# Kernel tuning notes

Measured on AMD Instinct MI355X. Metric: run time of the kernel, lower is better.

The kernel has to match this reference:

```python
import jax, jax.numpy as jnp
import numpy as np

H = 16
D_MODEL = 1024
D_K = D_MODEL // H


def setup_inputs() -> dict:
    key = jax.random.key(0)
    kx, kq, kk, kv, ko = jax.random.split(key, 5)
    B, T = 4, 2048
    scale = 1.0 / np.sqrt(D_MODEL)
    return {
        "X": jax.random.normal(kx, (B, T, D_MODEL), dtype=jnp.float32),
        "W_q": jax.random.normal(kq, (D_MODEL, D_MODEL), dtype=jnp.float32) * scale,
        "W_k": jax.random.normal(kk, (D_MODEL, D_MODEL), dtype=jnp.float32) * scale,
        "W_v": jax.random.normal(kv, (D_MODEL, D_MODEL), dtype=jnp.float32) * scale,
        "W_o": jax.random.normal(ko, (D_MODEL, D_MODEL), dtype=jnp.float32) * scale,
    }


def reference(X, W_q, W_k, W_v, W_o):
    B, T, D = X.shape
    # projections (torch Linear: x @ W.T); weights stored as [out, in]=[D,D]
    Q = (X @ W_q.T).reshape(B, T, H, D_K).transpose(0, 2, 1, 3)  # [B,H,T,Dk]
    K = (X @ W_k.T).reshape(B, T, H, D_K).transpose(0, 2, 1, 3)
    V = (X @ W_v.T).reshape(B, T, H, D_K).transpose(0, 2, 1, 3)
    S = jnp.einsum("bhqd,bhkd->bhqk", Q, K) * (D_K ** -0.5)  # [B,H,T,T]
    causal = jnp.tril(jnp.ones((T, T), dtype=bool))
    S = jnp.where(causal, S, -jnp.inf)
    A = jax.nn.softmax(S, axis=-1)
    out = jnp.einsum("bhqk,bhkd->bhqd", A, V)  # [B,H,T,Dk]
    out = out.transpose(0, 2, 1, 3).reshape(B, T, D)
    return out @ W_o.T
```

## Files before the change

### kernel.cpp

```cpp
#include <hip/hip_runtime.h>
#include <hip/hip_bf16.h>

#define T_SEQ 2048
#define NB 4
#define NH 16
#define DK 64
#define DM 1024
#define QKS 2048

typedef __attribute__((ext_vector_type(8))) __bf16 bf16x8;
typedef __attribute__((ext_vector_type(4))) __bf16 bf16x4;
typedef __attribute__((ext_vector_type(4))) float f32x4;
typedef __attribute__((ext_vector_type(2))) int i32x2;
typedef __attribute__((ext_vector_type(4))) int i32x4;

__device__ __forceinline__ void gl_lds16(const __bf16* g, __bf16* l) {
  __builtin_amdgcn_global_load_lds(
      (const __attribute__((address_space(1))) void*)g,
      (__attribute__((address_space(3))) void*)l,
      16, 0, 0);
}

__device__ __forceinline__ unsigned cvt_pk_bf16(float lo, float hi) {
  unsigned r;
  asm("v_cvt_pk_bf16_f32 %0, %1, %2" : "=v"(r) : "v"(lo), "v"(hi));
  return r;
}

__global__ __launch_bounds__(256) void cast_f32_to_bf16(const float* __restrict__ in,
                                                        __bf16* __restrict__ out, int n4) {
  int i = blockIdx.x * 256 + threadIdx.x;
  if (i >= n4) return;
  float4 v = reinterpret_cast<const float4*>(in)[i];
  bf16x4 o;
  o[0] = (__bf16)v.x; o[1] = (__bf16)v.y; o[2] = (__bf16)v.z; o[3] = (__bf16)v.w;
  reinterpret_cast<bf16x4*>(out)[i] = o;
}

__global__ __launch_bounds__(256) void cast_weights(const float* __restrict__ a,
                                                    const float* __restrict__ b,
                                                    const float* __restrict__ c,
                                                    const float* __restrict__ d,
                                                    __bf16* __restrict__ oa,
                                                    __bf16* __restrict__ ob,
                                                    __bf16* __restrict__ oc,
                                                    __bf16* __restrict__ od) {
  const int which = blockIdx.y;
  const float* in = (which == 0) ? a : (which == 1) ? b : (which == 2) ? c : d;
  __bf16* out = (which == 0) ? oa : (which == 1) ? ob : (which == 2) ? oc : od;
  int i = blockIdx.x * 256 + threadIdx.x;
  float4 v = reinterpret_cast<const float4*>(in)[i];
  bf16x4 o;
  o[0] = (__bf16)v.x; o[1] = (__bf16)v.y; o[2] = (__bf16)v.z; o[3] = (__bf16)v.w;
  reinterpret_cast<bf16x4*>(out)[i] = o;
}

template<typename CT, int MODE>
__global__ __launch_bounds__(256, 2) void gemm_nt(const __bf16* __restrict__ A,
                                                  const __bf16* __restrict__ B,
                                                  CT* __restrict__ C,
                                                  int M, int N, int K) {
  __shared__ alignas(16) __bf16 As[128][64];
  __shared__ alignas(16) __bf16 Bs[128][64];
  const int tid = threadIdx.x;
  const int m0 = blockIdx.y * 128, n0 = blockIdx.x * 128;
  const int w = tid >> 6, l = tid & 63, lg = l >> 4, lr = l & 15;
  const int wr = (w >> 1) * 64, wc = (w & 1) * 64;
  const int srow = l >> 3;
  const int schunk = (l & 7) ^ srow;

  f32x4 acc[4][4] = {};
  const int rsw = lr & 7;

  for (int k0 = 0; k0 < K; k0 += 64) {
    __syncthreads();
    #pragma unroll
    for (int j = 0; j < 4; ++j) {
      const int rbase = (w * 4 + j) * 8;
      gl_lds16(A + (size_t)(m0 + rbase + srow) * K + k0 + schunk * 8, &As[rbase][0]);
      gl_lds16(B + (size_t)(n0 + rbase + srow) * K + k0 + schunk * 8, &Bs[rbase][0]);
    }
    asm volatile("s_waitcnt vmcnt(0)" ::: "memory");
    __syncthreads();
    #pragma unroll
    for (int kk = 0; kk < 2; ++kk) {
      bf16x8 af[4], bfr[4];
      #pragma unroll
      for (int mt = 0; mt < 4; ++mt) {
        const char* p = (const char*)&As[wr + mt * 16 + lr][0];
        af[mt] = *reinterpret_cast<const bf16x8*>(p + (((kk * 4 + lg) ^ rsw) << 4));
      }
      #pragma unroll
      for (int nt = 0; nt < 4; ++nt) {
        const char* p = (const char*)&Bs[wc + nt * 16 + lr][0];
        bfr[nt] = *reinterpret_cast<const bf16x8*>(p + (((kk * 4 + lg) ^ rsw) << 4));
      }
      __builtin_amdgcn_s_setprio(1);
      #pragma unroll
      for (int mt = 0; mt < 4; ++mt)
        #pragma unroll
        for (int nt = 0; nt < 4; ++nt)
          acc[mt][nt] = __builtin_amdgcn_mfma_f32_16x16x32_bf16(af[mt], bfr[nt], acc[mt][nt], 0, 0, 0);
      __builtin_amdgcn_s_setprio(0);
    }
  }
  const float qsc = (MODE == 1 && n0 < 1024) ? 0.18033688f : 1.0f;
  #pragma unroll
  for (int mt = 0; mt < 4; ++mt)
    #pragma unroll
    for (int nt = 0; nt < 4; ++nt)
      #pragma unroll
      for (int r = 0; r < 4; ++r) {
        const int mg = m0 + wr + mt * 16 + 4 * lg + r;
        int ng = n0 + wc + nt * 16 + lr;
        if (MODE == 2)
          ng = (ng & ~31) | (8 * (lr >> 2) + (lr & 3) + ((nt & 1) << 2));
        float v = acc[mt][nt][r];
        if (MODE == 1) v *= qsc;
        C[(size_t)mg * N + ng] = (CT)v;
      }
}

__global__ __launch_bounds__(256, 3) void attn_fwd(const __bf16* __restrict__ QK,
                                                   const __bf16* __restrict__ VT,
                                                   __bf16* __restrict__ AO) {
  __shared__ alignas(16) __bf16 Ks[2][64][64];
  __shared__ alignas(16) __bf16 Vs[2][64][64];
  const int tid = threadIdx.x;
  const int w = tid >> 6, l = tid & 63, lg = l >> 4, lr = l & 15;

  const int fl = (int)blockIdx.x + 16 * (int)blockIdx.y;
  const int bh = ((fl & 7) << 3) | ((fl >> 3) & 7);
  const int qpair = fl >> 6;
  const int b = bh >> 4, h = bh & 15;
  const size_t bT = (size_t)b * T_SEQ;
  const int M = NB * T_SEQ;

  const int srow = l >> 3;
  const int schunk = (l & 7) ^ srow;
  const __bf16* Kg = QK + bT * QKS + 1024 + h * DK;
  const __bf16* Vg = VT + (size_t)(h * DK) * M + bT;
  const int rsw = lr & 7;

  const int qbA = qpair, qbB = 31 - qpair;
  const int qrwA = qbA * 64 + w * 16, qrwB = qbB * 64 + w * 16;
  const int klastA = qbA * 64, klastB = qbB * 64;

  const __bf16* QpA = QK + (bT + qrwA + lr) * QKS + h * DK;
  const __bf16* QpB = QK + (bT + qrwB + lr) * QKS + h * DK;
  const bf16x8 qfA0 = *reinterpret_cast<const bf16x8*>(QpA + 8 * lg);
  const bf16x8 qfA1 = *reinterpret_cast<const bf16x8*>(QpA + 32 + 8 * lg);
  const bf16x8 qfB0 = *reinterpret_cast<const bf16x8*>(QpB + 8 * lg);
  const bf16x8 qfB1 = *reinterpret_cast<const bf16x8*>(QpB + 32 + 8 * lg);

  f32x4 o_accA[4] = {}, o_accB[4] = {};
  float lsumA = 0.f, lsumB = 0.f;

  auto STAGE = [&](int buf, int kbase) {
    #pragma unroll
    for (int i = 0; i < 2; ++i) {
      const int seg = w * 2 + i;
      gl_lds16(Kg + (size_t)(kbase + seg * 8 + srow) * QKS + schunk * 8,
               &Ks[buf][seg * 8][0]);
      gl_lds16(Vg + (size_t)(seg * 8 + srow) * M + kbase + schunk * 8,
               &Vs[buf][seg * 8][0]);
    }
  };

  auto CHUNK = [&](const bf16x8& qf0, const bf16x8& qf1, f32x4* o_acc,
                   float& lsum, int qrw, bool masked, int k0,
                   const bf16x8* kf, const bf16x8* vf) {
    f32x4 s[4] = {};
    __builtin_amdgcn_s_setprio(1);
    #pragma unroll
    for (int ct = 0; ct < 4; ++ct) {
      s[ct] = __builtin_amdgcn_mfma_f32_16x16x32_bf16(kf[2 * ct], qf0, s[ct], 0, 0, 0);
      s[ct] = __builtin_amdgcn_mfma_f32_16x16x32_bf16(kf[2 * ct + 1], qf1, s[ct], 0, 0, 0);
    }
    __builtin_amdgcn_s_setprio(0);
    if (masked) {
      #pragma unroll
      for (int ct = 0; ct < 4; ++ct)
        #pragma unroll
        for (int r = 0; r < 4; ++r)
          if (k0 + 16 * ct + 4 * lg + r > qrw + lr) s[ct][r] = -1e30f;
    }
    unsigned pk[4][2];
    #pragma unroll
    for (int ct = 0; ct < 4; ++ct) {
      float p0 = exp2f(s[ct][0]), p1 = exp2f(s[ct][1]);
      float p2 = exp2f(s[ct][2]), p3 = exp2f(s[ct][3]);
      lsum += (p0 + p1) + (p2 + p3);
      pk[ct][0] = cvt_pk_bf16(p0, p1);
      pk[ct][1] = cvt_pk_bf16(p2, p3);
    }
    const bf16x8 pf0 = __builtin_bit_cast(bf16x8, i32x4{(int)pk[0][0], (int)pk[0][1],
                                                        (int)pk[1][0], (int)pk[1][1]});
    const bf16x8 pf1 = __builtin_bit_cast(bf16x8, i32x4{(int)pk[2][0], (int)pk[2][1],
                                                        (int)pk[3][0], (int)pk[3][1]});
    __builtin_amdgcn_s_setprio(1);
    #pragma unroll
    for (int dt = 0; dt < 4; ++dt) {
      o_acc[dt] = __builtin_amdgcn_mfma_f32_16x16x32_bf16(pf0, vf[2 * dt],     o_acc[dt], 0, 0, 0);
      o_acc[dt] = __builtin_amdgcn_mfma_f32_16x16x32_bf16(pf1, vf[2 * dt + 1], o_acc[dt], 0, 0, 0);
    }
    __builtin_amdgcn_s_setprio(0);
  };

  STAGE(0, 0);
  asm volatile("s_waitcnt vmcnt(0)" ::: "memory");
  __syncthreads();
  int buf = 0;

  for (int k0 = 0; k0 <= klastB; k0 += 64) {
    if (k0 + 64 <= klastB) STAGE(buf ^ 1, k0 + 64);

    bf16x8 kf[8], vf[8];
    #pragma unroll
    for (int ct = 0; ct < 4; ++ct) {
      const char* kb = (const char*)&Ks[buf][ct * 16 + lr][0];
      kf[2 * ct]     = *reinterpret_cast<const bf16x8*>(kb + ((lg ^ rsw) << 4));
      kf[2 * ct + 1] = *reinterpret_cast<const bf16x8*>(kb + (((lg + 4) ^ rsw) << 4));
      const char* vb = (const char*)&Vs[buf][ct * 16 + lr][0];
      vf[2 * ct]     = *reinterpret_cast<const bf16x8*>(vb + ((lg ^ rsw) << 4));
      vf[2 * ct + 1] = *reinterpret_cast<const bf16x8*>(vb + (((lg + 4) ^ rsw) << 4));
    }

    CHUNK(qfB0, qfB1, o_accB, lsumB, qrwB, k0 == klastB, k0, kf, vf);
    if (k0 <= klastA)
      CHUNK(qfA0, qfA1, o_accA, lsumA, qrwA, k0 == klastA, k0, kf, vf);

    asm volatile("s_waitcnt vmcnt(0)" ::: "memory");
    __syncthreads();
    buf ^= 1;
  }

  #pragma unroll
  for (int c = 0; c < 2; ++c) {
    const float lsum = c ? lsumA : lsumB;
    f32x4* oa = c ? o_accA : o_accB;
    const int qrw = c ? qrwA : qrwB;
    float v = lsum;
    v += __shfl_xor(v, 16);
    v += __shfl_xor(v, 32);
    const float linv = 1.0f / v;
    float inv[4];
    #pragma unroll
    for (int r = 0; r < 4; ++r) inv[r] = __shfl(linv, 4 * lg + r);
    #pragma unroll
    for (int dt = 0; dt < 4; ++dt)
      #pragma unroll
      for (int r = 0; r < 4; ++r) {
        const int rg = qrw + 4 * lg + r;
        const int cg = h * DK + dt * 16 + lr;
        AO[(bT + rg) * DM + cg] = (__bf16)(oa[dt][r] * inv[r]);
      }
  }
}

extern "C" void kernel_launch(void* const* d_in, const int* in_sizes, int n_in,
                              void* d_out, int out_size, void* d_ws, size_t ws_size,
                              hipStream_t stream) {
  (void)in_sizes; (void)n_in; (void)out_size; (void)ws_size;
  const float* X  = (const float*)d_in[0];
  const float* Wq = (const float*)d_in[1];
  const float* Wk = (const float*)d_in[2];
  const float* Wv = (const float*)d_in[3];
  const float* Wo = (const float*)d_in[4];
  float* OUT = (float*)d_out;

  char* ws = (char*)d_ws;
  const size_t SZ_X  = (size_t)NB * T_SEQ * DM * 2;
  const size_t SZ_W  = (size_t)DM * DM * 2;
  const size_t SZ_QK = (size_t)NB * T_SEQ * QKS * 2;
  __bf16* Xb  = (__bf16*)ws; ws += SZ_X;
  __bf16* Wqb = (__bf16*)ws; ws += SZ_W;
  __bf16* Wkb = (__bf16*)ws; ws += SZ_W;
  __bf16* Wvb = (__bf16*)ws; ws += SZ_W;
  __bf16* Wob = (__bf16*)ws; ws += SZ_W;
  __bf16* QKb = (__bf16*)ws; ws += SZ_QK;
  __bf16* VTb = (__bf16*)ws; ws += SZ_X;
  __bf16* AOb = (__bf16*)ws; ws += SZ_X;

  const int M = NB * T_SEQ;

  cast_f32_to_bf16<<<(M * DM / 4) / 256, 256, 0, stream>>>(X, Xb, M * DM / 4);
  cast_weights<<<dim3(DM * DM / 4 / 256, 4), 256, 0, stream>>>(Wq, Wk, Wv, Wo,
                                                               Wqb, Wkb, Wvb, Wob);

  gemm_nt<__bf16, 1><<<dim3(QKS / 128, M / 128), 256, 0, stream>>>(Xb, Wqb, QKb, M, QKS, DM);
  gemm_nt<__bf16, 2><<<dim3(M / 128, DM / 128), 256, 0, stream>>>(Wvb, Xb, VTb, DM, M, DM);
  attn_fwd<<<dim3(T_SEQ / 128, NB * NH), 256, 0, stream>>>(QKb, VTb, AOb);
  gemm_nt<float, 0><<<dim3(DM / 128, M / 128), 256, 0, stream>>>(AOb, Wob, OUT, M, DM, DM);
}
```

Before: 172.2 us.

## Process four query blocks per attention workgroup to share K/V tiles

Each attention workgroup now handles four causal query blocks (c, 15-c, 16+c, 31-c) instead of two, reusing every staged K/V tile across more query blocks and halving the grid to 512 workgroups. This cuts K/V global loads and LDS staging per unit of work while keeping per-block work balanced. In exchange it raises register pressure (launch bounds lowered from 3 to 2 waves per SIMD) and leaves fewer workgroups to fill the GPU.

```diff
diff --git a/kernel.cpp b/kernel.cpp
--- a/kernel.cpp
+++ b/kernel.cpp
@@ -121,7 +121,7 @@
       }
 }
 
-__global__ __launch_bounds__(256, 3) void attn_fwd(const __bf16* __restrict__ QK,
+__global__ __launch_bounds__(256, 2) void attn_fwd(const __bf16* __restrict__ QK,
                                                    const __bf16* __restrict__ VT,
                                                    __bf16* __restrict__ AO) {
   __shared__ alignas(16) __bf16 Ks[2][64][64];
@@ -129,9 +129,9 @@
   const int tid = threadIdx.x;
   const int w = tid >> 6, l = tid & 63, lg = l >> 4, lr = l & 15;
 
-  const int fl = (int)blockIdx.x + 16 * (int)blockIdx.y;
+  const int fl = (int)blockIdx.x + 8 * (int)blockIdx.y;
   const int bh = ((fl & 7) << 3) | ((fl >> 3) & 7);
-  const int qpair = fl >> 6;
+  const int c = fl >> 6;
   const int b = bh >> 4, h = bh & 15;
   const size_t bT = (size_t)b * T_SEQ;
   const int M = NB * T_SEQ;
@@ -142,19 +142,26 @@
   const __bf16* Vg = VT + (size_t)(h * DK) * M + bT;
   const int rsw = lr & 7;
 
-  const int qbA = qpair, qbB = 31 - qpair;
+  const int qbA = c, qbB = 15 - c, qbC = 16 + c, qbD = 31 - c;
   const int qrwA = qbA * 64 + w * 16, qrwB = qbB * 64 + w * 16;
-  const int klastA = qbA * 64, klastB = qbB * 64;
+  const int qrwC = qbC * 64 + w * 16, qrwD = qbD * 64 + w * 16;
+  const int klA = qbA * 64, klB = qbB * 64, klC = qbC * 64, klD = qbD * 64;
 
   const __bf16* QpA = QK + (bT + qrwA + lr) * QKS + h * DK;
   const __bf16* QpB = QK + (bT + qrwB + lr) * QKS + h * DK;
+  const __bf16* QpC = QK + (bT + qrwC + lr) * QKS + h * DK;
+  const __bf16* QpD = QK + (bT + qrwD + lr) * QKS + h * DK;
   const bf16x8 qfA0 = *reinterpret_cast<const bf16x8*>(QpA + 8 * lg);
   const bf16x8 qfA1 = *reinterpret_cast<const bf16x8*>(QpA + 32 + 8 * lg);
   const bf16x8 qfB0 = *reinterpret_cast<const bf16x8*>(QpB + 8 * lg);
   const bf16x8 qfB1 = *reinterpret_cast<const bf16x8*>(QpB + 32 + 8 * lg);
-
-  f32x4 o_accA[4] = {}, o_accB[4] = {};
-  float lsumA = 0.f, lsumB = 0.f;
+  const bf16x8 qfC0 = *reinterpret_cast<const bf16x8*>(QpC + 8 * lg);
+  const bf16x8 qfC1 = *reinterpret_cast<const bf16x8*>(QpC + 32 + 8 * lg);
+  const bf16x8 qfD0 = *reinterpret_cast<const bf16x8*>(QpD + 8 * lg);
+  const bf16x8 qfD1 = *reinterpret_cast<const bf16x8*>(QpD + 32 + 8 * lg);
+
+  f32x4 o_accA[4] = {}, o_accB[4] = {}, o_accC[4] = {}, o_accD[4] = {};
+  float lsumA = 0.f, lsumB = 0.f, lsumC = 0.f, lsumD = 0.f;
 
   auto STAGE = [&](int buf, int kbase) {
     #pragma unroll
@@ -212,8 +219,8 @@
   __syncthreads();
   int buf = 0;
 
-  for (int k0 = 0; k0 <= klastB; k0 += 64) {
-    if (k0 + 64 <= klastB) STAGE(buf ^ 1, k0 + 64);
+  for (int k0 = 0; k0 <= klD; k0 += 64) {
+    if (k0 + 64 <= klD) STAGE(buf ^ 1, k0 + 64);
 
     bf16x8 kf[8], vf[8];
     #pragma unroll
@@ -226,9 +233,10 @@
       vf[2 * ct + 1] = *reinterpret_cast<const bf16x8*>(vb + (((lg + 4) ^ rsw) << 4));
     }
 
-    CHUNK(qfB0, qfB1, o_accB, lsumB, qrwB, k0 == klastB, k0, kf, vf);
-    if (k0 <= klastA)
-      CHUNK(qfA0, qfA1, o_accA, lsumA, qrwA, k0 == klastA, k0, kf, vf);
+    CHUNK(qfD0, qfD1, o_accD, lsumD, qrwD, k0 == klD, k0, kf, vf);
+    if (k0 <= klC) CHUNK(qfC0, qfC1, o_accC, lsumC, qrwC, k0 == klC, k0, kf, vf);
+    if (k0 <= klB) CHUNK(qfB0, qfB1, o_accB, lsumB, qrwB, k0 == klB, k0, kf, vf);
+    if (k0 <= klA) CHUNK(qfA0, qfA1, o_accA, lsumA, qrwA, k0 == klA, k0, kf, vf);
 
     asm volatile("s_waitcnt vmcnt(0)" ::: "memory");
     __syncthreads();
@@ -236,10 +244,10 @@
   }
 
   #pragma unroll
-  for (int c = 0; c < 2; ++c) {
-    const float lsum = c ? lsumA : lsumB;
-    f32x4* oa = c ? o_accA : o_accB;
-    const int qrw = c ? qrwA : qrwB;
+  for (int cc = 0; cc < 4; ++cc) {
+    const float lsum = (cc == 0) ? lsumA : (cc == 1) ? lsumB : (cc == 2) ? lsumC : lsumD;
+    f32x4* oa = (cc == 0) ? o_accA : (cc == 1) ? o_accB : (cc == 2) ? o_accC : o_accD;
+    const int qrw = (cc == 0) ? qrwA : (cc == 1) ? qrwB : (cc == 2) ? qrwC : qrwD;
     float v = lsum;
     v += __shfl_xor(v, 16);
     v += __shfl_xor(v, 32);
@@ -290,6 +298,6 @@
 
   gemm_nt<__bf16, 1><<<dim3(QKS / 128, M / 128), 256, 0, stream>>>(Xb, Wqb, QKb, M, QKS, DM);
   gemm_nt<__bf16, 2><<<dim3(M / 128, DM / 128), 256, 0, stream>>>(Wvb, Xb, VTb, DM, M, DM);
-  attn_fwd<<<dim3(T_SEQ / 128, NB * NH), 256, 0, stream>>>(QKb, VTb, AOb);
+  attn_fwd<<<dim3(8, NB * NH), 256, 0, stream>>>(QKb, VTb, AOb);
   gemm_nt<float, 0><<<dim3(DM / 128, M / 128), 256, 0, stream>>>(AOb, Wob, OUT, M, DM, DM);
 }
```

Measured after the change: 162.5 us. 1.06x faster.
